# Kernel tuning notes

Measured on AMD Instinct MI355X. Metric: run time of the kernel, lower is better.

## Reference

```python
import jax, jax.numpy as jnp
import numpy as np

B, L, HID = 128, 256, 768
HID2 = 2 * HID
CDIM, SDIM, NPROJ = 192, 128, 128
FDIM = CDIM + SDIM + 1
BIG = 1e9  # finite pad so sorted invalid tokens go last without inf/nan issues


def setup_inputs() -> dict:
    key = jax.random.key(0)
    ks = jax.random.split(key, 12)
    H = jax.random.normal(ks[0], (B, L, HID), dtype=jnp.float32)
    tt = jax.random.randint(ks[1], (B, L), 0, 2, dtype=jnp.int32)
    m = jnp.ones((B, L), dtype=jnp.int32)
    s = 1.0 / np.sqrt(HID2)
    Wc = jax.random.uniform(ks[2], (CDIM, HID2), minval=-s, maxval=s, dtype=jnp.float32)
    bc = jax.random.uniform(ks[3], (CDIM,), minval=-s, maxval=s, dtype=jnp.float32)
    Ws = jax.random.uniform(ks[4], (SDIM, HID2), minval=-s, maxval=s, dtype=jnp.float32)
    bs = jax.random.uniform(ks[5], (SDIM,), minval=-s, maxval=s, dtype=jnp.float32)
    gate = jnp.array([0.5], dtype=jnp.float32)
    ln_g = jnp.ones((FDIM,), dtype=jnp.float32)
    ln_b = jnp.zeros((FDIM,), dtype=jnp.float32)
    sc = 1.0 / np.sqrt(FDIM)
    Wcls = jax.random.uniform(ks[6], (2, FDIM), minval=-sc, maxval=sc, dtype=jnp.float32)
    bcls = jax.random.uniform(ks[7], (2,), minval=-sc, maxval=sc, dtype=jnp.float32)
    d = jax.random.normal(ks[8], (NPROJ, HID), dtype=jnp.float32)
    proj_dirs = d / jnp.linalg.norm(d, axis=1, keepdims=True)
    return {"H": H, "tt": tt, "m": m, "Wc": Wc, "bc": bc, "Ws": Ws, "bs": bs,
            "gate": gate, "ln_g": ln_g, "ln_b": ln_b, "Wcls": Wcls, "bcls": bcls,
            "proj_dirs": proj_dirs}


def _forward(H, tt, m, Wc, bc, Ws, bs, gate, ln_g, ln_b, Wcls, bcls, proj_dirs):
    mask0 = (tt == 0) & (m == 1)  # [B,L]
    mask1 = (tt == 1) & (m == 1)
    f0 = mask0.astype(H.dtype)
    f1 = mask1.astype(H.dtype)
    cls = H[:, 0]  # [B,HID]
    mean0 = jnp.einsum('blh,bl->bh', H, f0) / jnp.clip(f0.sum(1, keepdims=True), 1.0)
    mean1 = jnp.einsum('blh,bl->bh', H, f1) / jnp.clip(f1.sum(1, keepdims=True), 1.0)
    rep = jnp.concatenate([cls, mean0 - mean1], axis=1)  # [B,2*HID]
    C = rep @ Wc.T + bc
    S = rep @ Ws.T + bs
    g = jax.nn.sigmoid(gate)  # [1]
    fused = jnp.concatenate([C * (1.0 - g), S * g], axis=1)

    # max-sliced W1 between token-type-0 and token-type-1 token sets, batched.
    P = jnp.einsum('blh,ph->blp', H, proj_dirs)  # [B,L,NPROJ]
    x0 = jnp.sort(jnp.where(mask0[..., None], P, BIG), axis=1)  # valid tokens first
    x1 = jnp.sort(jnp.where(mask1[..., None], P, BIG), axis=1)
    n0 = mask0.sum(1)
    n1 = mask1.sum(1)
    mcnt = jnp.minimum(n0, n1)  # [B]
    rmask = (jnp.arange(L)[None, :] < mcnt[:, None])[..., None]  # [B,L,1]
    diff = jnp.where(rmask, x0, 0.0) - jnp.where(rmask, x1, 0.0)
    mean_abs = jnp.abs(diff).sum(1) / jnp.maximum(mcnt, 1)[:, None].astype(P.dtype)  # [B,NPROJ]
    d_ot = mean_abs.max(axis=1, keepdims=True)  # [B,1]

    feat = jnp.concatenate([fused, d_ot], axis=1)  # [B,FDIM]
    mu = feat.mean(-1, keepdims=True)
    var = feat.var(-1, keepdims=True)
    normed = (feat - mu) * jax.lax.rsqrt(var + 1e-5) * ln_g + ln_b
    return normed @ Wcls.T + bcls  # [B,2]


def reference(H, tt, m, Wc, bc, Ws, bs, gate, ln_g, ln_b, Wcls, bcls, proj_dirs):
    return _forward(H, tt, m, Wc, bc, Ws, bs, gate, ln_g, ln_b, Wcls, bcls, proj_dirs)
```

## Files before the change

### kernel.cpp

```cpp
#include <hip/hip_runtime.h>
#include <cmath>

#define B_   128
#define L_   256
#define HID_ 768
#define HID2_ 1536
#define CDIM_ 192
#define SDIM_ 128
#define NPROJ_ 128
#define FDIM_ 321

typedef __attribute__((ext_vector_type(8))) short bf16x8;
typedef __attribute__((ext_vector_type(4))) float f32x4;

__device__ inline unsigned short bf_hi_trunc(float x) {
    return (unsigned short)(__float_as_uint(x) >> 16);
}
__device__ inline float bf2f(unsigned short s) {
    return __uint_as_float(((unsigned int)s) << 16);
}
__device__ inline unsigned short f2bf_rne(float x) {
    unsigned int u = __float_as_uint(x);
    unsigned int r = (u + 0x7fff + ((u >> 16) & 1)) >> 16;
    return (unsigned short)r;
}

__global__ __launch_bounds__(192) void pre_kernel(
    const float* __restrict__ Pd, unsigned short* __restrict__ Pjh,
    unsigned short* __restrict__ Pjl,
    const float* __restrict__ H, const int* __restrict__ tt,
    const int* __restrict__ mm, float* __restrict__ part)
{
    int tid = threadIdx.x;
    if (blockIdx.x < 128) {
        int i = blockIdx.x * 192 + tid;
        float4 v = ((const float4*)Pd)[i];
        ushort4 h, l;
        h.x = bf_hi_trunc(v.x); l.x = f2bf_rne(v.x - bf2f(h.x));
        h.y = bf_hi_trunc(v.y); l.y = f2bf_rne(v.y - bf2f(h.y));
        h.z = bf_hi_trunc(v.z); l.z = f2bf_rne(v.z - bf2f(h.z));
        h.w = bf_hi_trunc(v.w); l.w = f2bf_rne(v.w - bf2f(h.w));
        ((ushort4*)Pjh)[i] = h;
        ((ushort4*)Pjl)[i] = l;
        return;
    }
    int bid = blockIdx.x - 128;
    int b  = bid >> 3;
    int pr = bid & 7;

    __shared__ float sf0[32], sf1[32];
    if (tid < 32) {
        int l = pr * 32 + tid;
        int t = tt[b * L_ + l];
        int mv = mm[b * L_ + l];
        sf0[tid] = (t == 0 && mv == 1) ? 1.f : 0.f;
        sf1[tid] = (t == 1 && mv == 1) ? 1.f : 0.f;
    }
    __syncthreads();

    const float* Hb = H + ((size_t)(b * L_ + pr * 32)) * HID_;
    float4 a0 = make_float4(0.f, 0.f, 0.f, 0.f);
    float4 a1 = make_float4(0.f, 0.f, 0.f, 0.f);
    for (int l = 0; l < 32; ++l) {
        float4 x = *(const float4*)(Hb + (size_t)l * HID_ + tid * 4);
        float f0 = sf0[l], f1 = sf1[l];
        a0.x += x.x * f0; a0.y += x.y * f0; a0.z += x.z * f0; a0.w += x.w * f0;
        a1.x += x.x * f1; a1.y += x.y * f1; a1.z += x.z * f1; a1.w += x.w * f1;
    }
    float* dst = part + ((size_t)(b * 8 + pr)) * HID2_;
    *(float4*)(dst + tid * 4) = a0;
    *(float4*)(dst + HID_ + tid * 4) = a1;
}

#define LDSROW 72
__global__ __launch_bounds__(256, 4) void gemm_mfma(
    const float* __restrict__ H, const unsigned short* __restrict__ Pjh,
    const unsigned short* __restrict__ Pjl, float* __restrict__ Pt)
{
    __shared__ unsigned short Hs[2][64 * LDSROW];

    int tid = threadIdx.x;
    int w = tid >> 6;
    int lane = tid & 63;
    int c = lane & 15;
    int q = lane >> 4;

    int b = blockIdx.x >> 2;
    int lbase = (blockIdx.x & 3) * 64;

    const float* Hbase = H + ((size_t)(b * L_ + lbase)) * HID_;

    int hrow0 = tid >> 3;
    int hc4   = tid & 7;

    const unsigned short* pjh0 = Pjh + (size_t)(w * 32 + c) * HID_ + q * 8;
    const unsigned short* pjh1 = Pjh + (size_t)(w * 32 + 16 + c) * HID_ + q * 8;
    const unsigned short* pjl0 = Pjl + (size_t)(w * 32 + c) * HID_ + q * 8;
    const unsigned short* pjl1 = Pjl + (size_t)(w * 32 + 16 + c) * HID_ + q * 8;

    f32x4 acc[2][4] = {};

    float4 hreg[2];
    uint4 cah[2], cal[2];
    uint4 nah[2], nal[2];

    hreg[0] = *(const float4*)(Hbase + (size_t)hrow0 * HID_ + hc4 * 4);
    hreg[1] = *(const float4*)(Hbase + (size_t)(hrow0 + 32) * HID_ + hc4 * 4);
    cah[0] = *(const uint4*)(pjh0);
    cah[1] = *(const uint4*)(pjh1);
    cal[0] = *(const uint4*)(pjl0);
    cal[1] = *(const uint4*)(pjl1);
#pragma unroll
    for (int u = 0; u < 2; ++u) {
        int row = hrow0 + u * 32;
        float4 v = hreg[u];
        ushort4 h, l;
        h.x = bf_hi_trunc(v.x); l.x = f2bf_rne(v.x - bf2f(h.x));
        h.y = bf_hi_trunc(v.y); l.y = f2bf_rne(v.y - bf2f(h.y));
        h.z = bf_hi_trunc(v.z); l.z = f2bf_rne(v.z - bf2f(h.z));
        h.w = bf_hi_trunc(v.w); l.w = f2bf_rne(v.w - bf2f(h.w));
        *(ushort4*)&Hs[0][row * LDSROW + hc4 * 4]      = h;
        *(ushort4*)&Hs[0][row * LDSROW + 32 + hc4 * 4] = l;
    }
    __syncthreads();

    for (int it = 0; it < 24; ++it) {
        int cur = it & 1;
        int nxt = cur ^ 1;

        if (it + 1 < 24) {
            int k0 = (it + 1) * 32;
            hreg[0] = *(const float4*)(Hbase + (size_t)hrow0 * HID_ + k0 + hc4 * 4);
            hreg[1] = *(const float4*)(Hbase + (size_t)(hrow0 + 32) * HID_ + k0 + hc4 * 4);
            nah[0] = *(const uint4*)(pjh0 + k0);
            nah[1] = *(const uint4*)(pjh1 + k0);
            nal[0] = *(const uint4*)(pjl0 + k0);
            nal[1] = *(const uint4*)(pjl1 + k0);
        }

        bf16x8 bh[4], bl[4];
#pragma unroll
        for (int lt = 0; lt < 4; ++lt) {
            int l = lt * 16 + c;
            bh[lt] = *(const bf16x8*)&Hs[cur][l * LDSROW + q * 8];
            bl[lt] = *(const bf16x8*)&Hs[cur][l * LDSROW + 32 + q * 8];
        }
        bf16x8 ah[2], al[2];
        ah[0] = *(bf16x8*)&cah[0]; ah[1] = *(bf16x8*)&cah[1];
        al[0] = *(bf16x8*)&cal[0]; al[1] = *(bf16x8*)&cal[1];

#pragma unroll
        for (int pt = 0; pt < 2; ++pt)
#pragma unroll
        for (int lt = 0; lt < 4; ++lt) {
            acc[pt][lt] = __builtin_amdgcn_mfma_f32_16x16x32_bf16(ah[pt], bh[lt], acc[pt][lt], 0, 0, 0);
            acc[pt][lt] = __builtin_amdgcn_mfma_f32_16x16x32_bf16(ah[pt], bl[lt], acc[pt][lt], 0, 0, 0);
            acc[pt][lt] = __builtin_amdgcn_mfma_f32_16x16x32_bf16(al[pt], bh[lt], acc[pt][lt], 0, 0, 0);
        }

        if (it + 1 < 24) {
#pragma unroll
            for (int u = 0; u < 2; ++u) {
                int row = hrow0 + u * 32;
                float4 v = hreg[u];
                ushort4 h, l;
                h.x = bf_hi_trunc(v.x); l.x = f2bf_rne(v.x - bf2f(h.x));
                h.y = bf_hi_trunc(v.y); l.y = f2bf_rne(v.y - bf2f(h.y));
                h.z = bf_hi_trunc(v.z); l.z = f2bf_rne(v.z - bf2f(h.z));
                h.w = bf_hi_trunc(v.w); l.w = f2bf_rne(v.w - bf2f(h.w));
                *(ushort4*)&Hs[nxt][row * LDSROW + hc4 * 4]      = h;
                *(ushort4*)&Hs[nxt][row * LDSROW + 32 + hc4 * 4] = l;
            }
            cah[0] = nah[0]; cah[1] = nah[1];
            cal[0] = nal[0]; cal[1] = nal[1];
        }
        __syncthreads();
    }

#pragma unroll
    for (int pt = 0; pt < 2; ++pt)
#pragma unroll
    for (int lt = 0; lt < 4; ++lt)
#pragma unroll
    for (int r = 0; r < 4; ++r) {
        int p = w * 32 + pt * 16 + q * 4 + r;
        int l = lbase + lt * 16 + c;
        Pt[((size_t)(b * NPROJ_ + p)) * L_ + l] = acc[pt][lt][r];
    }
}

__global__ __launch_bounds__(256) void stats_fin(
    const float* __restrict__ H, const int* __restrict__ tt,
    const int* __restrict__ mm, const float* __restrict__ part,
    float* __restrict__ rep)
{
    int b = blockIdx.x;
    int tid = threadIdx.x;
    int t = tt[b * L_ + tid];
    int mv = mm[b * L_ + tid];
    int n0 = __syncthreads_count(t == 0 && mv == 1);
    int n1 = __syncthreads_count(t == 1 && mv == 1);
    float r0 = 1.f / fmaxf((float)n0, 1.f);
    float r1 = 1.f / fmaxf((float)n1, 1.f);

    const float* pp = part + (size_t)b * 8 * HID2_;
    for (int h = tid; h < HID_; h += 256) {
        float a0 = 0.f, a1 = 0.f;
#pragma unroll
        for (int q = 0; q < 8; ++q) {
            a0 += pp[(size_t)q * HID2_ + h];
            a1 += pp[(size_t)q * HID2_ + HID_ + h];
        }
        rep[(size_t)b * HID2_ + h] = H[(size_t)b * L_ * HID_ + h];
        rep[(size_t)b * HID2_ + HID_ + h] = a0 * r0 - a1 * r1;
    }
}

__global__ __launch_bounds__(256) void head_kernel(
    const float* __restrict__ rep, const float* __restrict__ Wc,
    const float* __restrict__ bc, const float* __restrict__ Ws,
    const float* __restrict__ bs, const float* __restrict__ gate,
    float* __restrict__ fused)
{
    __shared__ float srep[HID2_];

    int b = blockIdx.x >> 3;
    int ochunk = (blockIdx.x & 7) * 40;
    int tid = threadIdx.x;

    for (int i = tid; i < HID2_ / 4; i += 256)
        *(float4*)&srep[i * 4] = *(const float4*)&rep[(size_t)b * HID2_ + i * 4];
    __syncthreads();

    int w = tid >> 6;
    int lane = tid & 63;
    float g = 1.0f / (1.0f + expf(-gate[0]));

#pragma unroll
    for (int r = 0; r < 10; ++r) {
        int o = ochunk + r * 4 + w;
        bool isC = (o < CDIM_);
        const float4* wr = (const float4*)(isC ? (Wc + (size_t)o * HID2_)
                                               : (Ws + (size_t)(o - CDIM_) * HID2_));
        float acc = 0.f;
#pragma unroll
        for (int u = 0; u < 6; ++u) {
            int k4 = lane + u * 64;
            float4 a = *(const float4*)&srep[k4 * 4];
            float4 ww = wr[k4];
            acc += a.x * ww.x + a.y * ww.y + a.z * ww.z + a.w * ww.w;
        }
        for (int off = 32; off; off >>= 1) acc += __shfl_xor(acc, off, 64);
        if (lane == 0) {
            float bias = isC ? bc[o] : bs[o - CDIM_];
            float scale = isC ? (1.0f - g) : g;
            fused[(size_t)b * (CDIM_ + SDIM_) + o] = (acc + bias) * scale;
        }
    }
}

__global__ __launch_bounds__(256) void ot_kernel(
    const float* __restrict__ Pt, const int* __restrict__ tt,
    const int* __restrict__ mm, float* __restrict__ dist)
{
    int w = blockIdx.x * 4 + (threadIdx.x >> 6);
    int lane = threadIdx.x & 63;
    int b = w >> 7;
    int p = w & (NPROJ_ - 1);

    float4 pv = *(const float4*)(Pt + ((size_t)(b * NPROJ_ + p)) * L_ + lane * 4);
    int4 t4 = *(const int4*)(tt + (size_t)b * L_ + lane * 4);
    int4 m4 = *(const int4*)(mm + (size_t)b * L_ + lane * 4);

    float pvals[4] = {pv.x, pv.y, pv.z, pv.w};
    int tv[4] = {t4.x, t4.y, t4.z, t4.w};
    int mv[4] = {m4.x, m4.y, m4.z, m4.w};

    unsigned key[4];
#pragma unroll
    for (int r = 0; r < 4; ++r) {
        unsigned u = __float_as_uint(pvals[r]);
        unsigned s = (u & 0x80000000u) ? ~u : (u | 0x80000000u);
        unsigned label = (mv[r] == 1) ? (unsigned)tv[r] : 2u;
        key[r] = (s & ~3u) | label;
    }

    {
        unsigned mn0 = min(key[0], key[1]), mx0 = max(key[0], key[1]);
        key[0] = mn0; key[1] = mx0;
        unsigned mn1 = min(key[2], key[3]), mx1 = max(key[2], key[3]);
        key[2] = mx1; key[3] = mn1;
    }
#pragma unroll
    for (int k = 4; k <= 256; k <<= 1) {
        bool up = (lane & (k >> 2)) == 0;
#pragma unroll
        for (int j = k >> 1; j >= 4; j >>= 1) {
            int lj = j >> 2;
#pragma unroll
            for (int r = 0; r < 4; ++r) {
                unsigned o = (unsigned)__shfl_xor((int)key[r], lj, 64);
                bool lower = (lane & lj) == 0;
                unsigned mn = min(key[r], o), mx = max(key[r], o);
                key[r] = (lower == up) ? mn : mx;
            }
        }
        {
            unsigned mn0 = min(key[0], key[2]), mx0 = max(key[0], key[2]);
            key[0] = up ? mn0 : mx0; key[2] = up ? mx0 : mn0;
            unsigned mn1 = min(key[1], key[3]), mx1 = max(key[1], key[3]);
            key[1] = up ? mn1 : mx1; key[3] = up ? mx1 : mn1;
        }
        {
            unsigned mn0 = min(key[0], key[1]), mx0 = max(key[0], key[1]);
            key[0] = up ? mn0 : mx0; key[1] = up ? mx0 : mn0;
            unsigned mn1 = min(key[2], key[3]), mx1 = max(key[2], key[3]);
            key[2] = up ? mn1 : mx1; key[3] = up ? mx1 : mn1;
        }
    }

    int lab[4];
    float tval[4];
    unsigned sincl[4];
    unsigned run = 0;
#pragma unroll
    for (int r = 0; r < 4; ++r) {
        lab[r] = (int)(key[r] & 3u);
        unsigned s = key[r] & ~3u;
        unsigned u = (s & 0x80000000u) ? (s ^ 0x80000000u) : ~s;
        tval[r] = __uint_as_float(u);
        unsigned unit = ((lab[r] == 0) ? 0x10000u : 0u) | ((lab[r] == 1) ? 1u : 0u);
        run += unit;
        sincl[r] = run;
    }
    unsigned inc = run;
#pragma unroll
    for (int d = 1; d < 64; d <<= 1) {
        unsigned t = (unsigned)__shfl_up((int)inc, d, 64);
        if (lane >= d) inc += t;
    }
    unsigned ex = inc - run;
    unsigned total = (unsigned)__shfl((int)inc, 63, 64);
    int n0 = (int)(total >> 16), n1 = (int)(total & 0xffffu);
    int m = (n0 < n1) ? n0 : n1;

    float ssum = 0.f;
#pragma unroll
    for (int r = 0; r < 4; ++r) {
        unsigned C = ex + sincl[r];
        int c0 = (int)(C >> 16), c1 = (int)(C & 0xffffu);
        int s0 = (lab[r] == 0), s1 = (lab[r] == 1);
        int wi = abs(min(c0, m) - min(c1, m));
        int wp = abs(min(c0 - s0, m) - min(c1 - s1, m));
        ssum += tval[r] * (float)(wp - wi);
    }
    for (int off = 32; off; off >>= 1) ssum += __shfl_xor(ssum, off, 64);
    if (lane == 0) dist[b * NPROJ_ + p] = ssum / (float)((m > 1) ? m : 1);
}

__global__ __launch_bounds__(64) void final_kernel(
    const float* __restrict__ fused, const float* __restrict__ dist,
    const float* __restrict__ ln_g, const float* __restrict__ ln_b,
    const float* __restrict__ Wcls, const float* __restrict__ bcls,
    float* __restrict__ out)
{
    int b = blockIdx.x;
    int lane = threadIdx.x;

    float mx = fmaxf(dist[b * NPROJ_ + lane], dist[b * NPROJ_ + 64 + lane]);
    for (int off = 32; off; off >>= 1) mx = fmaxf(mx, __shfl_xor(mx, off, 64));

    float fv[6];
    float sum = 0.f, sq = 0.f;
#pragma unroll
    for (int u = 0; u < 6; ++u) {
        int j = lane + u * 64;
        float x = 0.f;
        if (j < CDIM_ + SDIM_) x = fused[(size_t)b * (CDIM_ + SDIM_) + j];
        else if (j == CDIM_ + SDIM_) x = mx;
        fv[u] = x;
        if (j < FDIM_) { sum += x; sq += x * x; }
    }
    for (int off = 32; off; off >>= 1) {
        sum += __shfl_xor(sum, off, 64);
        sq  += __shfl_xor(sq,  off, 64);
    }
    float mu = sum / (float)FDIM_;
    float var = sq / (float)FDIM_ - mu * mu;
    float inv = rsqrtf(var + 1e-5f);

    float d0 = 0.f, d1 = 0.f;
#pragma unroll
    for (int u = 0; u < 6; ++u) {
        int j = lane + u * 64;
        if (j < FDIM_) {
            float nx = (fv[u] - mu) * inv * ln_g[j] + ln_b[j];
            d0 += nx * Wcls[j];
            d1 += nx * Wcls[FDIM_ + j];
        }
    }
    for (int off = 32; off; off >>= 1) {
        d0 += __shfl_xor(d0, off, 64);
        d1 += __shfl_xor(d1, off, 64);
    }
    if (lane == 0) {
        out[b * 2 + 0] = d0 + bcls[0];
        out[b * 2 + 1] = d1 + bcls[1];
    }
}

extern "C" void kernel_launch(void* const* d_in, const int* in_sizes, int n_in,
                              void* d_out, int out_size, void* d_ws, size_t ws_size,
                              hipStream_t stream)
{
    const float* H    = (const float*)d_in[0];
    const int*   tt   = (const int*)d_in[1];
    const int*   mm   = (const int*)d_in[2];
    const float* Wc   = (const float*)d_in[3];
    const float* bc   = (const float*)d_in[4];
    const float* Ws   = (const float*)d_in[5];
    const float* bs   = (const float*)d_in[6];
    const float* gate = (const float*)d_in[7];
    const float* ln_g = (const float*)d_in[8];
    const float* ln_b = (const float*)d_in[9];
    const float* Wcls = (const float*)d_in[10];
    const float* bcls = (const float*)d_in[11];
    const float* Pd   = (const float*)d_in[12];
    float* out = (float*)d_out;

    float* ws = (float*)d_ws;
    float* Pt    = ws;
    float* part  = Pt + (size_t)B_ * NPROJ_ * L_;
    float* rep   = part + (size_t)B_ * 8 * HID2_;
    float* fused = rep + (size_t)B_ * HID2_;
    float* dist  = fused + (size_t)B_ * (CDIM_ + SDIM_);
    unsigned short* Pjh = (unsigned short*)(dist + (size_t)B_ * NPROJ_);
    unsigned short* Pjl = Pjh + (size_t)NPROJ_ * HID_;

    pre_kernel<<<128 + B_ * 8, 192, 0, stream>>>(Pd, Pjh, Pjl, H, tt, mm, part);
    gemm_mfma<<<B_ * 4, 256, 0, stream>>>(H, Pjh, Pjl, Pt);
    stats_fin<<<B_, 256, 0, stream>>>(H, tt, mm, part, rep);
    head_kernel<<<B_ * 8, 256, 0, stream>>>(rep, Wc, bc, Ws, bs, gate, fused);
    ot_kernel<<<B_ * NPROJ_ / 4, 256, 0, stream>>>(Pt, tt, mm, dist);
    final_kernel<<<B_, 64, 0, stream>>>(fused, dist, ln_g, ln_b, Wcls, bcls, out);
}
```

Baseline: 246.9 us.

## Fuse masked-mean stats into projection GEMM and merge head with OT kernel

Masked token sums are now accumulated inside the MFMA projection kernel from the H tiles it already loads, using shuffles and LDS atomics, so the separate full pass over H in pre_kernel goes away. Stats finalisation is folded into the head kernel, and the head and OT kernels share one launch, dropping two launches and the rep buffer round trip. In exchange the GEMM kernel uses more LDS and carries extra shuffle and atomic work, and its occupancy hint drops from 4 to 3 blocks.

```diff
diff --git a/kernel.cpp b/kernel.cpp
--- a/kernel.cpp
+++ b/kernel.cpp
@@ -27,57 +27,54 @@
 
 __global__ __launch_bounds__(192) void pre_kernel(
     const float* __restrict__ Pd, unsigned short* __restrict__ Pjh,
-    unsigned short* __restrict__ Pjl,
-    const float* __restrict__ H, const int* __restrict__ tt,
-    const int* __restrict__ mm, float* __restrict__ part)
-{
-    int tid = threadIdx.x;
-    if (blockIdx.x < 128) {
-        int i = blockIdx.x * 192 + tid;
-        float4 v = ((const float4*)Pd)[i];
-        ushort4 h, l;
-        h.x = bf_hi_trunc(v.x); l.x = f2bf_rne(v.x - bf2f(h.x));
-        h.y = bf_hi_trunc(v.y); l.y = f2bf_rne(v.y - bf2f(h.y));
-        h.z = bf_hi_trunc(v.z); l.z = f2bf_rne(v.z - bf2f(h.z));
-        h.w = bf_hi_trunc(v.w); l.w = f2bf_rne(v.w - bf2f(h.w));
-        ((ushort4*)Pjh)[i] = h;
-        ((ushort4*)Pjl)[i] = l;
-        return;
-    }
-    int bid = blockIdx.x - 128;
-    int b  = bid >> 3;
-    int pr = bid & 7;
-
-    __shared__ float sf0[32], sf1[32];
-    if (tid < 32) {
-        int l = pr * 32 + tid;
-        int t = tt[b * L_ + l];
-        int mv = mm[b * L_ + l];
-        sf0[tid] = (t == 0 && mv == 1) ? 1.f : 0.f;
-        sf1[tid] = (t == 1 && mv == 1) ? 1.f : 0.f;
-    }
-    __syncthreads();
-
-    const float* Hb = H + ((size_t)(b * L_ + pr * 32)) * HID_;
-    float4 a0 = make_float4(0.f, 0.f, 0.f, 0.f);
-    float4 a1 = make_float4(0.f, 0.f, 0.f, 0.f);
-    for (int l = 0; l < 32; ++l) {
-        float4 x = *(const float4*)(Hb + (size_t)l * HID_ + tid * 4);
-        float f0 = sf0[l], f1 = sf1[l];
-        a0.x += x.x * f0; a0.y += x.y * f0; a0.z += x.z * f0; a0.w += x.w * f0;
-        a1.x += x.x * f1; a1.y += x.y * f1; a1.z += x.z * f1; a1.w += x.w * f1;
-    }
-    float* dst = part + ((size_t)(b * 8 + pr)) * HID2_;
-    *(float4*)(dst + tid * 4) = a0;
-    *(float4*)(dst + HID_ + tid * 4) = a1;
+    unsigned short* __restrict__ Pjl)
+{
+    int i = blockIdx.x * 192 + threadIdx.x;
+    float4 v = ((const float4*)Pd)[i];
+    ushort4 h, l;
+    h.x = bf_hi_trunc(v.x); l.x = f2bf_rne(v.x - bf2f(h.x));
+    h.y = bf_hi_trunc(v.y); l.y = f2bf_rne(v.y - bf2f(h.y));
+    h.z = bf_hi_trunc(v.z); l.z = f2bf_rne(v.z - bf2f(h.z));
+    h.w = bf_hi_trunc(v.w); l.w = f2bf_rne(v.w - bf2f(h.w));
+    ((ushort4*)Pjh)[i] = h;
+    ((ushort4*)Pjl)[i] = l;
+}
+
+__device__ inline void stats_add(float4 x, float4 y,
+                                 float f0a, float f0b, float f1a, float f1b,
+                                 int colbase, int lane, float (*sacc)[HID_])
+{
+    float p0x = x.x * f0a + y.x * f0b, p0y = x.y * f0a + y.y * f0b;
+    float p0z = x.z * f0a + y.z * f0b, p0w = x.w * f0a + y.w * f0b;
+    float p1x = x.x * f1a + y.x * f1b, p1y = x.y * f1a + y.y * f1b;
+    float p1z = x.z * f1a + y.z * f1b, p1w = x.w * f1a + y.w * f1b;
+#pragma unroll
+    for (int off = 8; off < 64; off <<= 1) {
+        p0x += __shfl_xor(p0x, off, 64); p0y += __shfl_xor(p0y, off, 64);
+        p0z += __shfl_xor(p0z, off, 64); p0w += __shfl_xor(p0w, off, 64);
+        p1x += __shfl_xor(p1x, off, 64); p1y += __shfl_xor(p1y, off, 64);
+        p1z += __shfl_xor(p1z, off, 64); p1w += __shfl_xor(p1w, off, 64);
+    }
+    if (lane < 8) {
+        float* d0 = &sacc[0][colbase + lane * 4];
+        float* d1 = &sacc[1][colbase + lane * 4];
+        atomicAdd(d0 + 0, p0x); atomicAdd(d0 + 1, p0y);
+        atomicAdd(d0 + 2, p0z); atomicAdd(d0 + 3, p0w);
+        atomicAdd(d1 + 0, p1x); atomicAdd(d1 + 1, p1y);
+        atomicAdd(d1 + 2, p1z); atomicAdd(d1 + 3, p1w);
+    }
 }
 
 #define LDSROW 72
-__global__ __launch_bounds__(256, 4) void gemm_mfma(
+__global__ __launch_bounds__(256, 3) void gemm_mfma(
     const float* __restrict__ H, const unsigned short* __restrict__ Pjh,
-    const unsigned short* __restrict__ Pjl, float* __restrict__ Pt)
+    const unsigned short* __restrict__ Pjl, const int* __restrict__ tt,
+    const int* __restrict__ mm, float* __restrict__ Pt,
+    float* __restrict__ part)
 {
     __shared__ unsigned short Hs[2][64 * LDSROW];
+    __shared__ float sf0[64], sf1[64];
+    __shared__ float sacc[2][HID_];
 
     int tid = threadIdx.x;
     int w = tid >> 6;
@@ -92,6 +89,15 @@
 
     int hrow0 = tid >> 3;
     int hc4   = tid & 7;
+
+    if (tid < 64) {
+        int t  = tt[b * L_ + lbase + tid];
+        int mv = mm[b * L_ + lbase + tid];
+        sf0[tid] = (t == 0 && mv == 1) ? 1.f : 0.f;
+        sf1[tid] = (t == 1 && mv == 1) ? 1.f : 0.f;
+    }
+    for (int i = tid; i < 2 * HID_; i += 256)
+        (&sacc[0][0])[i] = 0.f;
 
     const unsigned short* pjh0 = Pjh + (size_t)(w * 32 + c) * HID_ + q * 8;
     const unsigned short* pjh1 = Pjh + (size_t)(w * 32 + 16 + c) * HID_ + q * 8;
@@ -123,6 +129,11 @@
         *(ushort4*)&Hs[0][row * LDSROW + 32 + hc4 * 4] = l;
     }
     __syncthreads();
+
+    float f0a = sf0[hrow0], f0b = sf0[hrow0 + 32];
+    float f1a = sf1[hrow0], f1b = sf1[hrow0 + 32];
+
+    stats_add(hreg[0], hreg[1], f0a, f0b, f1a, f1b, 0, lane, sacc);
 
     for (int it = 0; it < 24; ++it) {
         int cur = it & 1;
@@ -171,6 +182,8 @@
                 *(ushort4*)&Hs[nxt][row * LDSROW + hc4 * 4]      = h;
                 *(ushort4*)&Hs[nxt][row * LDSROW + 32 + hc4 * 4] = l;
             }
+            stats_add(hreg[0], hreg[1], f0a, f0b, f1a, f1b,
+                      (it + 1) * 32, lane, sacc);
             cah[0] = nah[0]; cah[1] = nah[1];
             cal[0] = nal[0]; cal[1] = nal[1];
         }
@@ -187,83 +200,75 @@
         int l = lbase + lt * 16 + c;
         Pt[((size_t)(b * NPROJ_ + p)) * L_ + l] = acc[pt][lt][r];
     }
-}
-
-__global__ __launch_bounds__(256) void stats_fin(
+
+    {
+        float* pdst = part + (size_t)(b * 4 + (blockIdx.x & 3)) * HID2_;
+        for (int i = tid; i < HID2_; i += 256)
+            pdst[i] = (&sacc[0][0])[i];
+    }
+}
+
+__global__ __launch_bounds__(256) void headot_kernel(
     const float* __restrict__ H, const int* __restrict__ tt,
     const int* __restrict__ mm, const float* __restrict__ part,
-    float* __restrict__ rep)
-{
-    int b = blockIdx.x;
-    int tid = threadIdx.x;
-    int t = tt[b * L_ + tid];
-    int mv = mm[b * L_ + tid];
-    int n0 = __syncthreads_count(t == 0 && mv == 1);
-    int n1 = __syncthreads_count(t == 1 && mv == 1);
-    float r0 = 1.f / fmaxf((float)n0, 1.f);
-    float r1 = 1.f / fmaxf((float)n1, 1.f);
-
-    const float* pp = part + (size_t)b * 8 * HID2_;
-    for (int h = tid; h < HID_; h += 256) {
-        float a0 = 0.f, a1 = 0.f;
-#pragma unroll
-        for (int q = 0; q < 8; ++q) {
-            a0 += pp[(size_t)q * HID2_ + h];
-            a1 += pp[(size_t)q * HID2_ + HID_ + h];
-        }
-        rep[(size_t)b * HID2_ + h] = H[(size_t)b * L_ * HID_ + h];
-        rep[(size_t)b * HID2_ + HID_ + h] = a0 * r0 - a1 * r1;
-    }
-}
-
-__global__ __launch_bounds__(256) void head_kernel(
-    const float* __restrict__ rep, const float* __restrict__ Wc,
-    const float* __restrict__ bc, const float* __restrict__ Ws,
-    const float* __restrict__ bs, const float* __restrict__ gate,
-    float* __restrict__ fused)
-{
-    __shared__ float srep[HID2_];
-
-    int b = blockIdx.x >> 3;
-    int ochunk = (blockIdx.x & 7) * 40;
-    int tid = threadIdx.x;
-
-    for (int i = tid; i < HID2_ / 4; i += 256)
-        *(float4*)&srep[i * 4] = *(const float4*)&rep[(size_t)b * HID2_ + i * 4];
-    __syncthreads();
-
-    int w = tid >> 6;
-    int lane = tid & 63;
-    float g = 1.0f / (1.0f + expf(-gate[0]));
-
-#pragma unroll
-    for (int r = 0; r < 10; ++r) {
-        int o = ochunk + r * 4 + w;
-        bool isC = (o < CDIM_);
-        const float4* wr = (const float4*)(isC ? (Wc + (size_t)o * HID2_)
-                                               : (Ws + (size_t)(o - CDIM_) * HID2_));
-        float acc = 0.f;
-#pragma unroll
-        for (int u = 0; u < 6; ++u) {
-            int k4 = lane + u * 64;
-            float4 a = *(const float4*)&srep[k4 * 4];
-            float4 ww = wr[k4];
-            acc += a.x * ww.x + a.y * ww.y + a.z * ww.z + a.w * ww.w;
-        }
-        for (int off = 32; off; off >>= 1) acc += __shfl_xor(acc, off, 64);
-        if (lane == 0) {
-            float bias = isC ? bc[o] : bs[o - CDIM_];
-            float scale = isC ? (1.0f - g) : g;
-            fused[(size_t)b * (CDIM_ + SDIM_) + o] = (acc + bias) * scale;
-        }
-    }
-}
-
-__global__ __launch_bounds__(256) void ot_kernel(
-    const float* __restrict__ Pt, const int* __restrict__ tt,
-    const int* __restrict__ mm, float* __restrict__ dist)
-{
-    int w = blockIdx.x * 4 + (threadIdx.x >> 6);
+    const float* __restrict__ Wc, const float* __restrict__ bc,
+    const float* __restrict__ Ws, const float* __restrict__ bs,
+    const float* __restrict__ gate, const float* __restrict__ Pt,
+    float* __restrict__ fused, float* __restrict__ dist)
+{
+    if (blockIdx.x < B_ * 8) {
+        __shared__ float srep[HID2_];
+        int b = blockIdx.x >> 3;
+        int ochunk = (blockIdx.x & 7) * 40;
+        int tid = threadIdx.x;
+
+        int t  = tt[b * L_ + tid];
+        int mv = mm[b * L_ + tid];
+        int n0 = __syncthreads_count(t == 0 && mv == 1);
+        int n1 = __syncthreads_count(t == 1 && mv == 1);
+        float r0 = 1.f / fmaxf((float)n0, 1.f);
+        float r1 = 1.f / fmaxf((float)n1, 1.f);
+
+        const float* pp = part + (size_t)b * 4 * HID2_;
+        for (int h = tid; h < HID_; h += 256) {
+            float a0 = pp[h] + pp[HID2_ + h] + pp[2 * HID2_ + h] + pp[3 * HID2_ + h];
+            float a1 = pp[HID_ + h] + pp[HID2_ + HID_ + h]
+                     + pp[2 * HID2_ + HID_ + h] + pp[3 * HID2_ + HID_ + h];
+            srep[h]        = H[(size_t)b * L_ * HID_ + h];
+            srep[HID_ + h] = a0 * r0 - a1 * r1;
+        }
+        __syncthreads();
+
+        int w = tid >> 6;
+        int lane = tid & 63;
+        float g = 1.0f / (1.0f + expf(-gate[0]));
+
+#pragma unroll
+        for (int r = 0; r < 10; ++r) {
+            int o = ochunk + r * 4 + w;
+            bool isC = (o < CDIM_);
+            const float4* wr = (const float4*)(isC ? (Wc + (size_t)o * HID2_)
+                                                   : (Ws + (size_t)(o - CDIM_) * HID2_));
+            float acc = 0.f;
+#pragma unroll
+            for (int u = 0; u < 6; ++u) {
+                int k4 = lane + u * 64;
+                float4 a = *(const float4*)&srep[k4 * 4];
+                float4 ww = wr[k4];
+                acc += a.x * ww.x + a.y * ww.y + a.z * ww.z + a.w * ww.w;
+            }
+            for (int off = 32; off; off >>= 1) acc += __shfl_xor(acc, off, 64);
+            if (lane == 0) {
+                float bias = isC ? bc[o] : bs[o - CDIM_];
+                float scale = isC ? (1.0f - g) : g;
+                fused[(size_t)b * (CDIM_ + SDIM_) + o] = (acc + bias) * scale;
+            }
+        }
+        return;
+    }
+
+    int bid = blockIdx.x - B_ * 8;
+    int w = bid * 4 + (threadIdx.x >> 6);
     int lane = threadIdx.x & 63;
     int b = w >> 7;
     int p = w & (NPROJ_ - 1);
@@ -336,8 +341,8 @@
     unsigned inc = run;
 #pragma unroll
     for (int d = 1; d < 64; d <<= 1) {
-        unsigned t = (unsigned)__shfl_up((int)inc, d, 64);
-        if (lane >= d) inc += t;
+        unsigned tt2 = (unsigned)__shfl_up((int)inc, d, 64);
+        if (lane >= d) inc += tt2;
     }
     unsigned ex = inc - run;
     unsigned total = (unsigned)__shfl((int)inc, 63, 64);
@@ -437,10 +442,9 @@
     unsigned short* Pjh = (unsigned short*)(dist + (size_t)B_ * NPROJ_);
     unsigned short* Pjl = Pjh + (size_t)NPROJ_ * HID_;
 
-    pre_kernel<<<128 + B_ * 8, 192, 0, stream>>>(Pd, Pjh, Pjl, H, tt, mm, part);
-    gemm_mfma<<<B_ * 4, 256, 0, stream>>>(H, Pjh, Pjl, Pt);
-    stats_fin<<<B_, 256, 0, stream>>>(H, tt, mm, part, rep);
-    head_kernel<<<B_ * 8, 256, 0, stream>>>(rep, Wc, bc, Ws, bs, gate, fused);
-    ot_kernel<<<B_ * NPROJ_ / 4, 256, 0, stream>>>(Pt, tt, mm, dist);
+    pre_kernel<<<128, 192, 0, stream>>>(Pd, Pjh, Pjl);
+    gemm_mfma<<<B_ * 4, 256, 0, stream>>>(H, Pjh, Pjl, tt, mm, Pt, part);
+    headot_kernel<<<B_ * 8 + B_ * NPROJ_ / 4, 256, 0, stream>>>(
+        H, tt, mm, part, Wc, bc, Ws, bs, gate, Pt, fused, dist);
     final_kernel<<<B_, 64, 0, stream>>>(fused, dist, ln_g, ln_b, Wcls, bcls, out);
 }
```

Result: faster. 230.8 us (-6.5%).
